# Optimization experiments

Hardware: AMD Instinct MI355X
Metric: run time of the kernel (lower is better)

Reference implementation:

```python
import jax, jax.numpy as jnp
import numpy as np

R = 9  # kernal for deep=1


def setup_inputs() -> dict:
    key = jax.random.key(0)
    ks = jax.random.split(key, 9)
    B, Cin, Cout, H, W = 4, 128, 128, 360, 360
    r2 = R * R
    x = jax.random.normal(ks[0], (B, Cin, H, W), dtype=jnp.float32)
    Wconv = jax.random.normal(ks[1], (Cout, Cin), dtype=jnp.float32) * 0.05
    bconv = jax.random.normal(ks[2], (Cout,), dtype=jnp.float32) * 0.05
    Wa = jax.random.normal(ks[3], (r2, r2), dtype=jnp.float32) * 0.05
    ba = jax.random.normal(ks[4], (r2,), dtype=jnp.float32) * 0.05
    Wb = jax.random.normal(ks[5], (r2, r2), dtype=jnp.float32) * 0.05
    bb = jax.random.normal(ks[6], (r2,), dtype=jnp.float32) * 0.05
    Wc = jax.random.normal(ks[7], (r2, r2), dtype=jnp.float32) * 0.05
    bc = jax.random.normal(ks[8], (r2,), dtype=jnp.float32) * 0.05
    return {"x": x, "Wconv": Wconv, "bconv": bconv,
            "Wa": Wa, "ba": ba, "Wb": Wb, "bb": bb, "Wc": Wc, "bc": bc}


def reference(x, Wconv, bconv, Wa, ba, Wb, bb, Wc, bc):
    r = R
    # 1x1 conv == channel-mixing matmul
    x = jnp.einsum('bchw,oc->bohw', x, Wconv) + bconv[None, :, None, None]
    B, C, H, W = x.shape
    padh = (-H) % r
    padw = (-W) % r
    x = jnp.pad(x, ((0, 0), (0, 0), (0, padh), (0, padw)))
    Hp, Wp = H + padh, W + padw
    h, w = Hp // r, Wp // r
    # rearrange 'b c (ch h) (cw w) -> b c (h w) (ch cw)', ch=cw=r
    x = x.reshape(B, C, r, h, r, w).transpose(0, 1, 3, 5, 2, 4).reshape(B, C, h * w, r * r)
    a = x @ Wa.T + ba
    b = x @ Wb.T + bb
    c = x @ Wc.T + bc
    # linear-attention trick: a @ (b^T @ c); b^T@c is (r^2, r^2) per (b,c)
    y = a @ (jnp.swapaxes(b, -1, -2) @ c) / r
    # inverse rearrange 'b c (h w) (ch cw) -> b c (ch h) (cw w)'
    y = y.reshape(B, C, h, w, r, r).transpose(0, 1, 4, 2, 5, 3).reshape(B, C, Hp, Wp)
    return y[:, :, :Hp - padh, :Wp - padw]
```

## Files before the change

kernel.cpp:

```cpp
#include <hip/hip_runtime.h>
#include <hip/hip_bf16.h>

typedef float f32x4 __attribute__((ext_vector_type(4)));
typedef short s16x8 __attribute__((ext_vector_type(8)));

#define DEVI __device__ __forceinline__

DEVI unsigned short f2bf(float f) {
    return __builtin_bit_cast(unsigned short, __float2bfloat16(f));
}


__global__ __launch_bounds__(256) void k_prep(
    const float* __restrict__ W, const float* __restrict__ Wa,
    const float* __restrict__ ba, const float* __restrict__ Wb,
    const float* __restrict__ bb, const float* __restrict__ Wc,
    const float* __restrict__ bc, unsigned short* __restrict__ Wbf,
    float* __restrict__ EAT, float* __restrict__ WCAT)
{
    const int tid = threadIdx.x, bid = blockIdx.x;
    if (bid < 64) {
        const int i = bid * 256 + tid;
        Wbf[i] = f2bf(W[i]);
        return;
    }
    const int out = (bid - 64) * 256 + tid;
    const int row = out / 96, col = out % 96;
    float ea = 0.f;
    if (row <= 81 && col <= 81) {
        for (int p = 0; p < 81; ++p) {
            const float wa = (col < 81) ? Wa[p * 81 + col] : ba[p];
            const float wb = (row < 81) ? Wb[p * 81 + row] : bb[p];
            ea += wa * wb;
        }
    }
    EAT[out] = ea;
    float wc = 0.f;
    if (col < 81) {
        if (row < 81) wc = Wc[col * 81 + row];
        else if (row == 81) wc = bc[col];
    }
    WCAT[out] = wc;
}

__global__ __launch_bounds__(256, 3) void k_conv(
    const float* __restrict__ x, const unsigned short* __restrict__ Wbf,
    const float* __restrict__ bcv, unsigned short* __restrict__ XR)
{
    __shared__ __align__(16) unsigned short Xs[160 * 136];
    const int tid = threadIdx.x;
    int bid = blockIdx.x;
    const int rb = bid % 10; bid /= 10;
    const int cw = bid % 9;  bid /= 9;
    const int ch = bid % 9;  const int b = bid / 9;
    const int H0 = ch * 40 + rb * 4, w0 = cw * 40;
    const int kfeat = ch * 9 + cw;
    const int t0 = rb * 160;

    const float* xb = x + (size_t)b * 128 * 129600;
    float4 va[5][4];
#pragma unroll
    for (int ii = 0; ii < 5; ++ii) {
        const int i = tid + ii * 256;
        const int cq = i / 40, nq = i % 40;
        const int hh = nq / 10, sub = nq % 10;
        const float* p = xb + (size_t)(cq * 4) * 129600 + (size_t)(H0 + hh) * 360 + w0 + sub * 4;
        va[ii][0] = *reinterpret_cast<const float4*>(p);
        va[ii][1] = *reinterpret_cast<const float4*>(p + 129600);
        va[ii][2] = *reinterpret_cast<const float4*>(p + 2 * 129600);
        va[ii][3] = *reinterpret_cast<const float4*>(p + 3 * 129600);
    }
#pragma unroll
    for (int ii = 0; ii < 5; ++ii) {
        const int i = tid + ii * 256;
        const int cq = i / 40, nq = i % 40;
        const int hh = nq / 10, sub = nq % 10;
        const int n0 = hh * 40 + sub * 4;
        const int cs = (cq ^ ((((n0 >> 2)) & 7) << 1)) * 4;
        const float4 v0 = va[ii][0], v1 = va[ii][1], v2 = va[ii][2], v3 = va[ii][3];
        ushort4 w0v = { f2bf(v0.x), f2bf(v1.x), f2bf(v2.x), f2bf(v3.x) };
        ushort4 w1v = { f2bf(v0.y), f2bf(v1.y), f2bf(v2.y), f2bf(v3.y) };
        ushort4 w2v = { f2bf(v0.z), f2bf(v1.z), f2bf(v2.z), f2bf(v3.z) };
        ushort4 w3v = { f2bf(v0.w), f2bf(v1.w), f2bf(v2.w), f2bf(v3.w) };
        *reinterpret_cast<ushort4*>(&Xs[(n0 + 0) * 136 + cs]) = w0v;
        *reinterpret_cast<ushort4*>(&Xs[(n0 + 1) * 136 + cs]) = w1v;
        *reinterpret_cast<ushort4*>(&Xs[(n0 + 2) * 136 + cs]) = w2v;
        *reinterpret_cast<ushort4*>(&Xs[(n0 + 3) * 136 + cs]) = w3v;
    }
    __syncthreads();

    const int lane = tid & 63, wid = tid >> 6;
    const int wm = wid >> 1, wn = wid & 1;
    const int lr = lane & 15, lg = lane >> 4;

    f32x4 acc[5][4] = {};
#pragma unroll
    for (int kk = 0; kk < 4; ++kk) {
        s16x8 xa[5], wb[4];
#pragma unroll
        for (int at = 0; at < 5; ++at) {
            const int n = wm * 80 + at * 16 + lr;
            const int cqs = ((kk * 8 + lg * 2) ^ (((n >> 2) & 7) << 1)) * 4;
            xa[at] = *reinterpret_cast<const s16x8*>(&Xs[n * 136 + cqs]);
        }
#pragma unroll
        for (int bt = 0; bt < 4; ++bt)
            wb[bt] = *reinterpret_cast<const s16x8*>(
                Wbf + (wn * 64 + bt * 16 + lr) * 128 + kk * 32 + lg * 8);
#pragma unroll
        for (int at = 0; at < 5; ++at)
#pragma unroll
            for (int bt = 0; bt < 4; ++bt)
                acc[at][bt] = __builtin_amdgcn_mfma_f32_16x16x32_bf16(xa[at], wb[bt], acc[at][bt], 0, 0, 0);
    }
#pragma unroll
    for (int bt = 0; bt < 4; ++bt) {
        const int o = wn * 64 + bt * 16 + lr;
        const float bias = bcv[o];
        unsigned short* dst = XR + (size_t)(b * 128 + o) * 129600 + (size_t)kfeat * 1600 + t0;
#pragma unroll
        for (int at = 0; at < 5; ++at) {
            const int n0 = wm * 80 + at * 16 + lg * 4;
            ushort4 hv = { f2bf(acc[at][bt][0] + bias), f2bf(acc[at][bt][1] + bias),
                           f2bf(acc[at][bt][2] + bias), f2bf(acc[at][bt][3] + bias) };
            *reinterpret_cast<ushort4*>(&dst[n0]) = hv;
        }
    }
}

__global__ __launch_bounds__(256) void k_gram(
    const unsigned short* __restrict__ XR, float* __restrict__ G2)
{
    __shared__ __align__(16) unsigned short Rs[96 * 168];
    const int tid = threadIdx.x;
    const int half = blockIdx.x & 1, bo = blockIdx.x >> 1;
    for (int i = 81 * 168 + tid; i < 96 * 168; i += 256)
        Rs[i] = (i < 82 * 168) ? (unsigned short)0x3F80 : (unsigned short)0;
    const unsigned short* Rg = XR + (size_t)bo * 129600;
    const int lane = tid & 63, wid = tid >> 6;
    const int wm = wid >> 1, wn = wid & 1;
    const int lr = lane & 15, lg = lane >> 4;
    f32x4 acc[3][3] = {};
    for (int it = 0; it < 5; ++it) {
        const int t0 = half * 800 + it * 160;
        __syncthreads();
        for (int i = tid; i < 81 * 20; i += 256) {
            const int r = i / 20, g = i % 20;
            *reinterpret_cast<s16x8*>(&Rs[r * 168 + g * 8]) =
                *reinterpret_cast<const s16x8*>(Rg + (size_t)r * 1600 + t0 + g * 8);
        }
        __syncthreads();
#pragma unroll
        for (int kk = 0; kk < 5; ++kk) {
            const int koff = kk * 32 + lg * 8;
            s16x8 af[3], bfr[3];
#pragma unroll
            for (int mt = 0; mt < 3; ++mt)
                af[mt] = *reinterpret_cast<const s16x8*>(&Rs[(wm * 48 + mt * 16 + lr) * 168 + koff]);
#pragma unroll
            for (int nt = 0; nt < 3; ++nt)
                bfr[nt] = *reinterpret_cast<const s16x8*>(&Rs[(wn * 48 + nt * 16 + lr) * 168 + koff]);
#pragma unroll
            for (int mt = 0; mt < 3; ++mt)
#pragma unroll
                for (int nt = 0; nt < 3; ++nt)
                    acc[mt][nt] = __builtin_amdgcn_mfma_f32_16x16x32_bf16(af[mt], bfr[nt], acc[mt][nt], 0, 0, 0);
        }
    }
    float* Gb = G2 + (size_t)(half * 512 + bo) * 9216;
#pragma unroll
    for (int mt = 0; mt < 3; ++mt)
#pragma unroll
        for (int nt = 0; nt < 3; ++nt)
#pragma unroll
            for (int rg = 0; rg < 4; ++rg) {
                const int row = wm * 48 + mt * 16 + lg * 4 + rg;
                const int col = wn * 48 + nt * 16 + lr;
                Gb[row * 96 + col] = acc[mt][nt][rg];
            }
}

__global__ __launch_bounds__(256) void k_small(
    const float* __restrict__ G2, const float* __restrict__ EAT,
    const float* __restrict__ WCAT, unsigned short* __restrict__ NT)
{
    __shared__ float Gs[96 * 98];
    __shared__ float Us[96 * 98];
    const int tid = threadIdx.x;
    const int bo = blockIdx.x;
    const int ty = tid >> 4, tx = tid & 15;
    const int r0 = ty * 6, q0 = tx * 6;

    const float* Gg0 = G2 + (size_t)bo * 9216;
    const float* Gg1 = G2 + (size_t)(512 + bo) * 9216;
    for (int i = tid; i < 96 * 96; i += 256) {
        const int r = i / 96, c = i % 96;
        Gs[r * 98 + c] = Gg0[i] + Gg1[i];
    }
    __syncthreads();

    {
        float acc[6][6] = {};
        for (int l = 0; l <= 81; ++l) {
            float gv[6], wv[6];
#pragma unroll
            for (int a = 0; a < 6; ++a) gv[a] = Gs[l * 98 + r0 + a];
#pragma unroll
            for (int b2 = 0; b2 < 6; ++b2) wv[b2] = WCAT[l * 96 + q0 + b2];
#pragma unroll
            for (int a = 0; a < 6; ++a)
#pragma unroll
                for (int b2 = 0; b2 < 6; ++b2)
                    acc[a][b2] += gv[a] * wv[b2];
        }
#pragma unroll
        for (int a = 0; a < 6; ++a)
#pragma unroll
            for (int b2 = 0; b2 < 6; ++b2)
                Us[(r0 + a) * 98 + q0 + b2] = acc[a][b2];
    }
    __syncthreads();

    float acc[6][6] = {};
    for (int j = 0; j <= 81; ++j) {
        float ev[6], uv[6];
#pragma unroll
        for (int a = 0; a < 6; ++a) ev[a] = EAT[j * 96 + r0 + a];
#pragma unroll
        for (int b2 = 0; b2 < 6; ++b2) uv[b2] = Us[j * 98 + q0 + b2];
#pragma unroll
        for (int a = 0; a < 6; ++a)
#pragma unroll
            for (int b2 = 0; b2 < 6; ++b2)
                acc[a][b2] += ev[a] * uv[b2];
    }
    unsigned short* NTb = NT + (size_t)bo * 9216;
#pragma unroll
    for (int b2 = 0; b2 < 6; ++b2)
#pragma unroll
        for (int a = 0; a < 6; ++a)
            NTb[(q0 + b2) * 96 + (r0 + a)] = f2bf(acc[a][b2] * (1.f / 9.f));
}

__global__ __launch_bounds__(256) void k_apply(
    const unsigned short* __restrict__ XR, const unsigned short* __restrict__ NT,
    float* __restrict__ out)
{
    __shared__ __align__(16) unsigned short Xs[160 * 104];
    const int tid = threadIdx.x;
    const int bid = blockIdx.x;
    const int fifth = bid % 5, bo = bid / 5;
    for (int i = tid; i < 160 * 15; i += 256) {
        const int t = i / 15, k = 81 + i % 15;
        Xs[t * 104 + k] = (k == 81) ? (unsigned short)0x3F80 : (unsigned short)0;
    }
    const int lane = tid & 63, wid = tid >> 6;
    const int wm = wid >> 1, wn = wid & 1;
    const int lr = lane & 15, lg = lane >> 4;

    const unsigned short* NTb = NT + (size_t)bo * 9216;
    s16x8 nb[3][3];
#pragma unroll
    for (int qt = 0; qt < 3; ++qt)
#pragma unroll
        for (int kk = 0; kk < 3; ++kk)
            nb[qt][kk] = *reinterpret_cast<const s16x8*>(
                NTb + (wn * 48 + qt * 16 + lr) * 96 + kk * 32 + lg * 8);

    const unsigned short* Rg = XR + (size_t)bo * 129600;
    float* ob = out + (size_t)bo * 129600;

    for (int it = 0; it < 2; ++it) {
        const int t0 = fifth * 320 + it * 160;
        __syncthreads();
        for (int i = tid; i < 81 * 20; i += 256) {
            const int k = i % 81, g = i / 81;
            const s16x8 v = *reinterpret_cast<const s16x8*>(Rg + (size_t)k * 1600 + t0 + g * 8);
#pragma unroll
            for (int e = 0; e < 8; ++e)
                Xs[(g * 8 + e) * 104 + k] = (unsigned short)v[e];
        }
        __syncthreads();
        f32x4 acc[5][3] = {};
#pragma unroll
        for (int kk = 0; kk < 3; ++kk) {
            s16x8 xa[5];
#pragma unroll
            for (int at = 0; at < 5; ++at)
                xa[at] = *reinterpret_cast<const s16x8*>(
                    &Xs[(wm * 80 + at * 16 + lr) * 104 + kk * 32 + lg * 8]);
#pragma unroll
            for (int at = 0; at < 5; ++at)
#pragma unroll
                for (int qt = 0; qt < 3; ++qt)
                    acc[at][qt] = __builtin_amdgcn_mfma_f32_16x16x32_bf16(xa[at], nb[qt][kk], acc[at][qt], 0, 0, 0);
        }
#pragma unroll
        for (int qt = 0; qt < 3; ++qt) {
            const int q = wn * 48 + qt * 16 + lr;
            if (q < 81) {
                const int chq = q / 9, cwq = q % 9;
                float* oq = ob + (size_t)chq * 40 * 360 + cwq * 40;
#pragma unroll
                for (int at = 0; at < 5; ++at) {
                    const int tt = t0 + wm * 80 + at * 16 + lg * 4;
                    const int hh = tt / 40, ww = tt % 40;
                    *reinterpret_cast<f32x4*>(&oq[hh * 360 + ww]) = acc[at][qt];
                }
            }
        }
    }
}

extern "C" void kernel_launch(void* const* d_in, const int* in_sizes, int n_in,
                              void* d_out, int out_size, void* d_ws, size_t ws_size,
                              hipStream_t stream)
{
    (void)in_sizes; (void)n_in; (void)out_size; (void)ws_size;
    const float* x   = (const float*)d_in[0];
    const float* Wcv = (const float*)d_in[1];
    const float* bcv = (const float*)d_in[2];
    const float* Wa  = (const float*)d_in[3];
    const float* ba  = (const float*)d_in[4];
    const float* Wb  = (const float*)d_in[5];
    const float* bbv = (const float*)d_in[6];
    const float* Wc  = (const float*)d_in[7];
    const float* bc2 = (const float*)d_in[8];
    float* out = (float*)d_out;

    char* w = (char*)d_ws;
    unsigned short* XR = (unsigned short*)w;
    float* G2 = (float*)(w + 132710400ull);
    unsigned short* NT = (unsigned short*)(w + 170459136ull);
    unsigned short* Wbf = (unsigned short*)(w + 179896320ull);
    float* EAT  = (float*)(w + 179929088ull);
    float* WCAT = (float*)(w + 179965952ull);

    k_prep <<<100,  256, 0, stream>>>(Wcv, Wa, ba, Wb, bbv, Wc, bc2, Wbf, EAT, WCAT);
    k_conv <<<3240, 256, 0, stream>>>(x, Wbf, bcv, XR);
    k_gram <<<1024, 256, 0, stream>>>(XR, G2);
    k_small<<<512,  256, 0, stream>>>(G2, EAT, WCAT, NT);
    k_apply<<<2560, 256, 0, stream>>>(XR, NT, out);
}
```

Baseline: 325.4 us.

## Stage conv output through LDS for coalesced stores; swizzle transposed tile in apply

The conv kernel now writes its bf16 results into shared memory, then copies them out as 16-byte coalesced stores per output row instead of scattered 8-byte stores. The apply kernel's transpose into LDS now packs four features per 8-byte write into an XOR-swizzled 128-wide row layout, replacing scalar 2-byte writes, and the MFMA operand reads use the matching swizzle. This targets uncoalesced global writes and LDS bank conflicts and store count, at the cost of extra barriers and shared memory reuse in the conv kernel.

```diff
diff --git a/kernel.cpp b/kernel.cpp
--- a/kernel.cpp
+++ b/kernel.cpp
@@ -113,18 +113,27 @@
             for (int bt = 0; bt < 4; ++bt)
                 acc[at][bt] = __builtin_amdgcn_mfma_f32_16x16x32_bf16(xa[at], wb[bt], acc[at][bt], 0, 0, 0);
     }
+    __syncthreads();
 #pragma unroll
     for (int bt = 0; bt < 4; ++bt) {
         const int o = wn * 64 + bt * 16 + lr;
         const float bias = bcv[o];
-        unsigned short* dst = XR + (size_t)(b * 128 + o) * 129600 + (size_t)kfeat * 1600 + t0;
 #pragma unroll
         for (int at = 0; at < 5; ++at) {
             const int n0 = wm * 80 + at * 16 + lg * 4;
             ushort4 hv = { f2bf(acc[at][bt][0] + bias), f2bf(acc[at][bt][1] + bias),
                            f2bf(acc[at][bt][2] + bias), f2bf(acc[at][bt][3] + bias) };
-            *reinterpret_cast<ushort4*>(&dst[n0]) = hv;
-        }
+            *reinterpret_cast<ushort4*>(&Xs[o * 168 + n0]) = hv;
+        }
+    }
+    __syncthreads();
+    unsigned short* dstb = XR + (size_t)b * 128 * 129600 + (size_t)kfeat * 1600 + t0;
+#pragma unroll
+    for (int j = 0; j < 10; ++j) {
+        const int item = tid + j * 256;
+        const int o = item / 20, s2 = item % 20;
+        *reinterpret_cast<s16x8*>(dstb + (size_t)o * 129600 + s2 * 8) =
+            *reinterpret_cast<const s16x8*>(&Xs[o * 168 + s2 * 8]);
     }
 }
 
@@ -246,13 +255,19 @@
     const unsigned short* __restrict__ XR, const unsigned short* __restrict__ NT,
     float* __restrict__ out)
 {
-    __shared__ __align__(16) unsigned short Xs[160 * 104];
+    __shared__ __align__(16) unsigned short Xs[160 * 128];
     const int tid = threadIdx.x;
-    const int bid = blockIdx.x;
-    const int fifth = bid % 5, bo = bid / 5;
-    for (int i = tid; i < 160 * 15; i += 256) {
-        const int t = i / 15, k = 81 + i % 15;
-        Xs[t * 104 + k] = (k == 81) ? (unsigned short)0x3F80 : (unsigned short)0;
+    const int fifth = blockIdx.x % 5, bo = blockIdx.x / 5;
+    for (int i = tid; i < 320; i += 256) {
+        const int t = i >> 1, h = i & 1;
+        const int s = (t >> 3) & 7;
+        const ushort4 z = { 0, 0, 0, 0 };
+        if (h == 0) {
+            *reinterpret_cast<ushort4*>(&Xs[t * 128 + ((10 ^ s) << 3) + 4]) = z;
+        } else {
+            *reinterpret_cast<ushort4*>(&Xs[t * 128 + ((11 ^ s) << 3)]) = z;
+            *reinterpret_cast<ushort4*>(&Xs[t * 128 + ((11 ^ s) << 3) + 4]) = z;
+        }
     }
     const int lane = tid & 63, wid = tid >> 6;
     const int wm = wid >> 1, wn = wid & 1;
@@ -273,12 +288,33 @@
     for (int it = 0; it < 2; ++it) {
         const int t0 = fifth * 320 + it * 160;
         __syncthreads();
-        for (int i = tid; i < 81 * 20; i += 256) {
-            const int k = i % 81, g = i / 81;
-            const s16x8 v = *reinterpret_cast<const s16x8*>(Rg + (size_t)k * 1600 + t0 + g * 8);
-#pragma unroll
-            for (int e = 0; e < 8; ++e)
-                Xs[(g * 8 + e) * 104 + k] = (unsigned short)v[e];
+        for (int i = tid; i < 420; i += 256) {
+            const int kq = i / 20, g = i % 20;
+            if (kq < 20) {
+                const unsigned short* src = Rg + (size_t)(4 * kq) * 1600 + t0 + g * 8;
+                const s16x8 v0 = *reinterpret_cast<const s16x8*>(src);
+                const s16x8 v1 = *reinterpret_cast<const s16x8*>(src + 1600);
+                const s16x8 v2 = *reinterpret_cast<const s16x8*>(src + 3200);
+                const s16x8 v3 = *reinterpret_cast<const s16x8*>(src + 4800);
+                const int colb = (((kq >> 1) ^ (g & 7)) << 3) + ((kq & 1) << 2);
+#pragma unroll
+                for (int e = 0; e < 8; ++e) {
+                    const int t = g * 8 + e;
+                    ushort4 wv = { (unsigned short)v0[e], (unsigned short)v1[e],
+                                   (unsigned short)v2[e], (unsigned short)v3[e] };
+                    *reinterpret_cast<ushort4*>(&Xs[t * 128 + colb]) = wv;
+                }
+            } else {
+                const s16x8 v = *reinterpret_cast<const s16x8*>(
+                    Rg + (size_t)80 * 1600 + t0 + g * 8);
+                const int colb = (10 ^ (g & 7)) << 3;
+#pragma unroll
+                for (int e = 0; e < 8; ++e) {
+                    const int t = g * 8 + e;
+                    ushort4 wv = { (unsigned short)v[e], (unsigned short)0x3F80, 0, 0 };
+                    *reinterpret_cast<ushort4*>(&Xs[t * 128 + colb]) = wv;
+                }
+            }
         }
         __syncthreads();
         f32x4 acc[5][3] = {};
@@ -286,9 +322,12 @@
         for (int kk = 0; kk < 3; ++kk) {
             s16x8 xa[5];
 #pragma unroll
-            for (int at = 0; at < 5; ++at)
+            for (int at = 0; at < 5; ++at) {
+                const int t = wm * 80 + at * 16 + lr;
+                const int s = (t >> 3) & 7;
                 xa[at] = *reinterpret_cast<const s16x8*>(
-                    &Xs[(wm * 80 + at * 16 + lr) * 104 + kk * 32 + lg * 8]);
+                    &Xs[t * 128 + (((kk * 4 + lg) ^ s) << 3)]);
+            }
 #pragma unroll
             for (int at = 0; at < 5; ++at)
 #pragma unroll
```

Measured after the change: 305.5 us (median of 2 runs). 1.07x faster.
